# Kernel optimization log

Measured on AMD Instinct MI355X. Metric: run time of the kernel, lower is better.

## Reference

```python
import jax, jax.numpy as jnp
import numpy as np

B, S, H, R = 32, 1024, 1024, 53
EPS = 1e-12
ATT_EPS = 1e10


def setup_inputs() -> dict:
    key = jax.random.key(0)
    ks = jax.random.split(key, 20)
    sc = 0.02
    n = lambda k, shape: jax.random.normal(k, shape, jnp.float32) * sc
    return {
        "relation": jax.random.randint(ks[0], (B, 1), 0, R),
        "last_hidden_size": jax.random.normal(ks[1], (B, S, H), jnp.float32),
        "sub_head": jax.random.randint(ks[2], (B, 1), 0, S),
        "sub_tail": jax.random.randint(ks[3], (B, 1), 0, S),
        "attention_mask": jax.random.randint(ks[4], (B, S), 0, 2).astype(jnp.int32),
        # learned params
        "rel_emb": n(ks[5], (R, H)),
        "Wrf": n(ks[6], (H, H)), "brf": jnp.zeros((H,), jnp.float32),
        "cln_w": jnp.ones((H,), jnp.float32), "cln_b": jnp.zeros((H,), jnp.float32),
        "Wwd": n(ks[7], (H, 2 * H)), "Wbd": n(ks[8], (H, 2 * H)),
        "Wq": n(ks[9], (H, H)), "bq": jnp.zeros((H,), jnp.float32),
        "Wk": n(ks[10], (H, H)), "bk": jnp.zeros((H,), jnp.float32),
        "Wv": n(ks[11], (H, H)), "bv": jnp.zeros((H,), jnp.float32),
        "Wo": n(ks[12], (1, H)), "bo": jnp.zeros((1,), jnp.float32),
    }


def reference(relation, last_hidden_size, sub_head, sub_tail, attention_mask,
              rel_emb, Wrf, brf, cln_w, cln_b, Wwd, Wbd,
              Wq, bq, Wk, bk, Wv, bv, Wo, bo):
    x = last_hidden_size  # [B,S,H]; dropout is identity at inference
    # relation feature: embedding -> linear -> ReLU6
    rel = jnp.clip(jnp.einsum('boh,gh->bog', rel_emb[relation], Wrf) + brf, 0.0, 6.0)  # [B,1,H]
    # gather subject head/tail token features
    bidx = jnp.arange(x.shape[0])[:, None]
    sub = (x[bidx, sub_head] + x[bidx, sub_tail]) * 0.5  # [B,1,H]
    cond = jnp.concatenate([rel, sub], axis=-1)  # [B,1,2H]
    # conditional layer norm: per-example weight/bias generated from cond
    w = jnp.einsum('boc,gc->bog', cond, Wwd) + cln_w  # [B,1,H]
    b = jnp.einsum('boc,gc->bog', cond, Wbd) + cln_b  # [B,1,H]
    mean = jnp.mean(x, axis=-1, keepdims=True)
    c = x - mean
    var = jnp.mean(c * c, axis=-1, keepdims=True)
    normed = c / jnp.sqrt(var + EPS) * w + b  # [B,S,H]
    # ReLU-activated QKV attention with additive mask bias and residual
    q = jax.nn.relu(jnp.einsum('bsh,gh->bsg', normed, Wq) + bq)
    k = jax.nn.relu(jnp.einsum('bsh,gh->bsg', normed, Wk) + bk)
    v = jax.nn.relu(jnp.einsum('bsh,gh->bsg', normed, Wv) + bv)
    e = jnp.einsum('bsh,bth->bst', q, k)  # [B,S,S]
    m = attention_mask.astype(e.dtype)[:, None, :]  # [B,1,S]
    e = e - ATT_EPS * (1.0 - m)
    a = jax.nn.softmax(e, axis=-1)
    hidden = jnp.einsum('bst,bth->bsh', a, v) + normed  # [B,S,H]
    pred_obj_head = (jnp.einsum('bsh,gh->bsg', hidden, Wo) + bo)[..., 0]  # [B,S]
    return (pred_obj_head, hidden)
```

## Files before the change

kernel.cpp:

```cpp
#include <hip/hip_runtime.h>
#include <hip/hip_bf16.h>

#define NB 32
#define NS 1024
#define NH 1024

typedef short s16x4 __attribute__((ext_vector_type(4)));
typedef short s16x8 __attribute__((ext_vector_type(8)));
typedef float f32x4 __attribute__((ext_vector_type(4)));

typedef __attribute__((address_space(3))) void lds_void;
typedef const __attribute__((address_space(1))) void gmem_void;

__device__ __forceinline__ short f2bf(float f) {
  __hip_bfloat16 h = __float2bfloat16(f);
  return *reinterpret_cast<short*>(&h);
}
__device__ __forceinline__ float bf2f(short s) {
  union { unsigned u; float f; } cv;
  cv.u = ((unsigned)(unsigned short)s) << 16;
  return cv.f;
}

__device__ __forceinline__ float wave_reduce_sum(float v) {
#pragma unroll
  for (int o = 32; o; o >>= 1) v += __shfl_xor(v, o);
  return v;
}
__device__ __forceinline__ float wave_reduce_max(float v) {
#pragma unroll
  for (int o = 32; o; o >>= 1) v = fmaxf(v, __shfl_xor(v, o));
  return v;
}
__device__ __forceinline__ float block_reduce_sum(float v, float* red) {
  v = wave_reduce_sum(v);
  __syncthreads();
  if ((threadIdx.x & 63) == 0) red[threadIdx.x >> 6] = v;
  __syncthreads();
  return red[0] + red[1] + red[2] + red[3];
}
__device__ __forceinline__ float block_reduce_max(float v, float* red) {
  v = wave_reduce_max(v);
  __syncthreads();
  if ((threadIdx.x & 63) == 0) red[threadIdx.x >> 6] = v;
  __syncthreads();
  return fmaxf(fmaxf(red[0], red[1]), fmaxf(red[2], red[3]));
}


#define BAR1 do { __builtin_amdgcn_s_barrier();                              \
                  asm volatile("s_waitcnt lgkmcnt(0)" ::: "memory");         \
                  __builtin_amdgcn_sched_barrier(0); } while (0)
#define BAR2 do { __builtin_amdgcn_s_barrier();                              \
                  asm volatile("" ::: "memory"); } while (0)
#define VW   asm volatile("s_waitcnt vmcnt(4)" ::: "memory")
#define VW2  asm volatile("s_waitcnt vmcnt(2)" ::: "memory")

#define GEMM_PRE()                                                           \
  const int tid  = threadIdx.x;                                              \
  const int lane = tid & 63;                                                 \
  const int w    = tid >> 6;                                                 \
  const int wm   = w >> 2, wn = w & 3;                                       \
  const int fr   = lane & 15, fq = lane >> 4;                                \
  const long tA  = (long)(tid >> 3) * 1024 +                                 \
                   (((tid & 7) ^ ((tid >> 3) & 7)) << 3);                    \
  const int kc0  = (fq * 8) ^ ((fr & 7) * 8);                                \
  const int kc1  = (fq * 8 + 32) ^ ((fr & 7) * 8);                           \
  const int rdA  = wm * 8192 + fr * 64;                                      \
  const int rdB  = 16384 + (wn >> 1) * 8192 + (wn & 1) * 4096 + fr * 64;     \
  const int wsl  = w * 512;                                                  \
  f32x4 acc[8][4];                                                           \
  s16x8 aF[2][4][2], bF[2][2][2];                                            \
  _Pragma("unroll") for (int i_ = 0; i_ < 8; ++i_)                           \
    _Pragma("unroll") for (int j_ = 0; j_ < 4; ++j_)                         \
      acc[i_][j_] = (f32x4){0.f, 0.f, 0.f, 0.f};

#define STAGE(d, isB, h, kt)                                                 \
  do {                                                                       \
    const short* _g = ((isB) ? gB + (n0 + (h) * 128) * 1024                  \
                             : gA + (m0 + (h) * 128) * 1024) +               \
                      (long)((kt) & 15) * 64 + tA;                           \
    short* _l = lds + (d) * 32768 + (isB) * 16384 + (h) * 8192 + wsl;        \
    __builtin_amdgcn_global_load_lds((gmem_void*)_g, (lds_void*)_l,          \
                                     16, 0, 0);                              \
    __builtin_amdgcn_global_load_lds((gmem_void*)(_g + 65536),               \
                                     (lds_void*)(_l + 4096), 16, 0, 0);      \
  } while (0)

#define RD_A(d, mq)                                                          \
  _Pragma("unroll") for (int mi = 0; mi < 4; ++mi) {                         \
    aF[mq][mi][0] = *(const s16x8*)(lds + (d) * 32768 + rdA + (mq) * 4096 +  \
                                    mi * 1024 + kc0);                        \
    aF[mq][mi][1] = *(const s16x8*)(lds + (d) * 32768 + rdA + (mq) * 4096 +  \
                                    mi * 1024 + kc1);                        \
  }
#define RD_B(d, nq)                                                          \
  _Pragma("unroll") for (int ni = 0; ni < 2; ++ni) {                         \
    bF[nq][ni][0] = *(const s16x8*)(lds + (d) * 32768 + rdB + (nq) * 2048 +  \
                                    ni * 1024 + kc0);                        \
    bF[nq][ni][1] = *(const s16x8*)(lds + (d) * 32768 + rdB + (nq) * 2048 +  \
                                    ni * 1024 + kc1);                        \
  }
#define MMA(mq, nq)                                                          \
  do {                                                                       \
    __builtin_amdgcn_s_setprio(1);                                           \
    _Pragma("unroll") for (int kk = 0; kk < 2; ++kk)                         \
      _Pragma("unroll") for (int mi = 0; mi < 4; ++mi)                       \
        _Pragma("unroll") for (int ni = 0; ni < 2; ++ni)                     \
          acc[(mq) * 4 + mi][(nq) * 2 + ni] =                                \
              __builtin_amdgcn_mfma_f32_16x16x32_bf16(                       \
                  aF[mq][mi][kk], bF[nq][ni][kk],                            \
                  acc[(mq) * 4 + mi][(nq) * 2 + ni], 0, 0, 0);               \
    __builtin_amdgcn_s_setprio(0);                                           \
  } while (0)

#define GEMM_MAIN()                                                          \
  GEMM_PRE();                                                                \
  STAGE(0, 1, 0, 0); STAGE(0, 1, 1, 0); STAGE(0, 0, 0, 0); STAGE(0, 0, 1, 0);\
  STAGE(1, 1, 0, 1); STAGE(1, 1, 1, 1);                                      \
  VW; BAR2;                                                                  \
  RD_A(0, 0);                                                                \
  for (int it = 0; it < 8; ++it) {                                           \
    const int t1 = 2 * it + 1, t2 = 2 * it + 2, t3 = 2 * it + 3;             \
    RD_B(0, 0); STAGE(1, 0, 0, t1); BAR1; MMA(0, 0); BAR2;                   \
    RD_B(0, 1); STAGE(1, 0, 1, t1); BAR1; MMA(0, 1); BAR2;                   \
    RD_A(0, 1); STAGE(0, 1, 0, t2); BAR1; MMA(1, 1); BAR2;                   \
    VW2;        STAGE(0, 1, 1, t2); BAR1; RD_A(1, 0); MMA(1, 0); BAR2;       \
    RD_B(1, 0); STAGE(0, 0, 0, t2); BAR1; MMA(0, 0); BAR2;                   \
    RD_B(1, 1); STAGE(0, 0, 1, t2); BAR1; MMA(0, 1); BAR2;                   \
    RD_A(1, 1); STAGE(1, 1, 0, t3); BAR1; MMA(1, 1); BAR2;                   \
    VW2;        STAGE(1, 1, 1, t3); BAR1; RD_A(0, 0); MMA(1, 0); BAR2;       \
  }


__global__ __launch_bounds__(256) void prep_kernel(const int* __restrict__ relation,
    const float* __restrict__ x, const int* __restrict__ sub_head,
    const int* __restrict__ sub_tail, const float* __restrict__ rel_emb,
    const float* __restrict__ Wrf, const float* __restrict__ brf,
    float* __restrict__ cond,
    const float* __restrict__ Wq, const float* __restrict__ Wk,
    const float* __restrict__ Wv, short* __restrict__ wout) {
  const int blk = blockIdx.x;
  const int tid = threadIdx.x;
  if (blk >= 1056) {
    long i = ((long)(blk - 1056) * 256 + tid) * 4;
    int seg = (int)(i >> 20);
    long off = i & 1048575;
    const float* src = seg == 0 ? Wq : (seg == 1 ? Wk : Wv);
    f32x4 v = *(const f32x4*)(src + off);
    s16x4 o = { f2bf(v[0]), f2bf(v[1]), f2bf(v[2]), f2bf(v[3]) };
    *(s16x4*)(wout + i) = o;
    return;
  }
  if (blk >= 1024) {
    const int b = blk - 1024;
    const int sh = sub_head[b], st = sub_tail[b];
    for (int h = tid * 4; h < NH; h += 1024) {
      f32x4 a = *(const f32x4*)(x + ((long)b * NS + sh) * NH + h);
      f32x4 c = *(const f32x4*)(x + ((long)b * NS + st) * NH + h);
      f32x4 o = { 0.5f * (a[0] + c[0]), 0.5f * (a[1] + c[1]),
                  0.5f * (a[2] + c[2]), 0.5f * (a[3] + c[3]) };
      *(f32x4*)(cond + b * 2 * NH + NH + h) = o;
    }
    return;
  }
  const int g = blk;
  __shared__ float wr[NH];
  for (int h = tid * 4; h < NH; h += 1024)
    *(f32x4*)(wr + h) = *(const f32x4*)(Wrf + (long)g * NH + h);
  __syncthreads();
  const int lane = tid & 63, wid = tid >> 6;
  const float bg = brf[g];
  for (int b = wid; b < NB; b += 4) {
    const int rid = relation[b];
    const float* re = rel_emb + (long)rid * NH;
    float s = 0.f;
#pragma unroll
    for (int h = lane * 4; h < NH; h += 256) {
      f32x4 rv = *(const f32x4*)(re + h);
      f32x4 wv = *(const f32x4*)(wr + h);
      s += rv[0] * wv[0] + rv[1] * wv[1] + rv[2] * wv[2] + rv[3] * wv[3];
    }
    s = wave_reduce_sum(s);
    if (lane == 0) cond[b * 2 * NH + g] = fminf(fmaxf(s + bg, 0.f), 6.f);
  }
}

__global__ __launch_bounds__(256) void wb_kernel(const float* __restrict__ cond,
    const float* __restrict__ Wwd, const float* __restrict__ Wbd,
    const float* __restrict__ cln_w, const float* __restrict__ cln_b,
    float* __restrict__ wln, float* __restrict__ bln) {
  const int g = blockIdx.x;
  const int tid = threadIdx.x;
  __shared__ float wrow[2 * NH];
  __shared__ float brow[2 * NH];
  for (int i = tid * 4; i < 2 * NH; i += 1024) {
    *(f32x4*)(wrow + i) = *(const f32x4*)(Wwd + (long)g * 2 * NH + i);
    *(f32x4*)(brow + i) = *(const f32x4*)(Wbd + (long)g * 2 * NH + i);
  }
  __syncthreads();
  const int lane = tid & 63, wid = tid >> 6;
  const float cw = cln_w[g], cb = cln_b[g];
  for (int b = wid; b < NB; b += 4) {
    float sw = 0.f, sb = 0.f;
#pragma unroll
    for (int c = lane * 4; c < 2 * NH; c += 256) {
      f32x4 cv = *(const f32x4*)(cond + b * 2 * NH + c);
      f32x4 wv = *(const f32x4*)(wrow + c);
      f32x4 bv = *(const f32x4*)(brow + c);
      sw += cv[0] * wv[0] + cv[1] * wv[1] + cv[2] * wv[2] + cv[3] * wv[3];
      sb += cv[0] * bv[0] + cv[1] * bv[1] + cv[2] * bv[2] + cv[3] * bv[3];
    }
    sw = wave_reduce_sum(sw);
    sb = wave_reduce_sum(sb);
    if (lane == 0) {
      wln[b * NH + g] = sw + cw;
      bln[b * NH + g] = sb + cb;
    }
  }
}

__global__ __launch_bounds__(256) void ln_kernel(const float* __restrict__ x,
    const float* __restrict__ wln, const float* __restrict__ bln, short* __restrict__ normed) {
  const long row = blockIdx.x;
  const int tid = threadIdx.x;
  const long b = row >> 10;
  __shared__ float red[4];
  f32x4 v = *(const f32x4*)(x + row * NH + tid * 4);
  float mean = block_reduce_sum(v[0] + v[1] + v[2] + v[3], red) * (1.f / NH);
  float c0 = v[0] - mean, c1 = v[1] - mean, c2 = v[2] - mean, c3 = v[3] - mean;
  float var = block_reduce_sum(c0 * c0 + c1 * c1 + c2 * c2 + c3 * c3, red) * (1.f / NH);
  float rstd = rsqrtf(var + 1e-12f);
  f32x4 wv = *(const f32x4*)(wln + b * NH + tid * 4);
  f32x4 bv = *(const f32x4*)(bln + b * NH + tid * 4);
  s16x4 o = { f2bf(c0 * rstd * wv[0] + bv[0]), f2bf(c1 * rstd * wv[1] + bv[1]),
              f2bf(c2 * rstd * wv[2] + bv[2]), f2bf(c3 * rstd * wv[3] + bv[3]) };
  *(s16x4*)(normed + row * NH + tid * 4) = o;
}

__global__ __launch_bounds__(512, 2) void qkv_kernel(const short* __restrict__ A,
    const short* __restrict__ Wqkv,
    const float* __restrict__ bq, const float* __restrict__ bk, const float* __restrict__ bv,
    short* __restrict__ q, short* __restrict__ k, short* __restrict__ vT) {
  __shared__ short lds[67584];
  const int flat = blockIdx.y * 12 + blockIdx.x;
  const int gid  = (flat & 7) * 192 + (flat >> 3);
  const int mt = gid / 12, nt = gid % 12;
  const short* gA = A;
  const short* gB = Wqkv;
  const long n0 = (long)nt * 256;
  const long m0 = (long)mt * 256;
  GEMM_MAIN();
  const int z = nt >> 2;
  const long hc0 = (long)(nt & 3) * 256;
  const float* bias = z == 0 ? bq : (z == 1 ? bk : bv);
  if (z < 2) {
    short* dst = z == 0 ? q : k;
#pragma unroll
    for (int nI = 0; nI < 4; ++nI) {
      const long col = hc0 + wn * 64 + nI * 16 + fr;
      const float bcol = bias[col];
#pragma unroll
      for (int mI = 0; mI < 8; ++mI)
#pragma unroll
        for (int r = 0; r < 4; ++r) {
          const long row = m0 + wm * 128 + mI * 16 + fq * 4 + r;
          dst[row * NH + col] = f2bf(fmaxf(acc[mI][nI][r] + bcol, 0.f));
        }
    }
  } else {
    asm volatile("s_waitcnt vmcnt(0)" ::: "memory");
    __syncthreads();
#pragma unroll
    for (int nI = 0; nI < 4; ++nI) {
      const int hl = wn * 64 + nI * 16 + fr;
      const float bcol = bias[hc0 + hl];
#pragma unroll
      for (int mI = 0; mI < 8; ++mI) {
        const int tl = wm * 128 + mI * 16 + fq * 4;
        s16x4 pk = { f2bf(fmaxf(acc[mI][nI][0] + bcol, 0.f)),
                     f2bf(fmaxf(acc[mI][nI][1] + bcol, 0.f)),
                     f2bf(fmaxf(acc[mI][nI][2] + bcol, 0.f)),
                     f2bf(fmaxf(acc[mI][nI][3] + bcol, 0.f)) };
        *(s16x4*)(lds + hl * 264 + tl) = pk;
      }
    }
    __syncthreads();
    const int h = tid >> 1, half = tid & 1;
    const long bb = m0 >> 10;
    short* dst = vT + ((bb * NH) + hc0 + h) * NS + (m0 & 1023) + half * 128;
    const short* src = lds + h * 264 + half * 128;
#pragma unroll
    for (int j = 0; j < 16; ++j)
      *(s16x8*)(dst + j * 8) = *(const s16x8*)(src + j * 8);
  }
}

__global__ __launch_bounds__(512, 2) void escore_kernel(const short* __restrict__ q,
    const short* __restrict__ k, const int* __restrict__ amask, float* __restrict__ e) {
  __shared__ short lds[65536];
  const int flat = blockIdx.z * 16 + blockIdx.y * 4 + blockIdx.x;
  const int gid  = (flat & 7) * 64 + (flat >> 3);
  const int b = gid >> 4, mt = (gid >> 2) & 3, nt = gid & 3;
  const short* gA = q + (long)b * NS * NH;
  const short* gB = k + (long)b * NS * NH;
  const long m0 = (long)mt * 256;
  const long n0 = (long)nt * 256;
  GEMM_MAIN();
  float* eb = e + (long)b * NS * NS;
#pragma unroll
  for (int mI = 0; mI < 8; ++mI)
#pragma unroll
    for (int nI = 0; nI < 4; ++nI) {
      const long col = n0 + wn * 64 + nI * 16 + fr;
      const float mb = -1e10f * (1.f - (float)amask[b * NS + col]);
#pragma unroll
      for (int r = 0; r < 4; ++r) {
        const long row = m0 + wm * 128 + mI * 16 + fq * 4 + r;
        eb[row * NS + col] = acc[mI][nI][r] + mb;
      }
    }
}

__global__ __launch_bounds__(256) void softmax_kernel(const float* __restrict__ e,
    short* __restrict__ a, float* __restrict__ inv_sum) {
  const long row = blockIdx.x;
  const int tid = threadIdx.x;
  __shared__ float red[4];
  f32x4 v = *(const f32x4*)(e + row * NS + tid * 4);
  float m = block_reduce_max(fmaxf(fmaxf(v[0], v[1]), fmaxf(v[2], v[3])), red);
  float p0 = expf(v[0] - m), p1 = expf(v[1] - m);
  float p2 = expf(v[2] - m), p3 = expf(v[3] - m);
  float s = block_reduce_sum(p0 + p1 + p2 + p3, red);
  s16x4 o = { f2bf(p0), f2bf(p1), f2bf(p2), f2bf(p3) };
  *(s16x4*)(a + row * NS + tid * 4) = o;
  if (tid == 0) inv_sum[row] = 1.f / s;
}

__global__ __launch_bounds__(512, 2) void av_kernel(const short* __restrict__ a,
    const short* __restrict__ vT, const float* __restrict__ inv_sum,
    const short* __restrict__ normed, const float* __restrict__ Wo,
    float* __restrict__ hid, float* __restrict__ pred_part) {
  __shared__ short lds[65536];
  const int flat = blockIdx.z * 16 + blockIdx.y * 4 + blockIdx.x;
  const int gid  = (flat & 7) * 64 + (flat >> 3);
  const int b = gid >> 4, mt = (gid >> 2) & 3, nt = gid & 3;
  const short* gA = a + (long)b * NS * NS;
  const short* gB = vT + (long)b * NH * NS;
  const long m0 = (long)mt * 256;
  const long n0 = (long)nt * 256;
  GEMM_MAIN();
  float pp[8][4];
#pragma unroll
  for (int mI = 0; mI < 8; ++mI)
#pragma unroll
    for (int r = 0; r < 4; ++r) pp[mI][r] = 0.f;
#pragma unroll
  for (int nI = 0; nI < 4; ++nI) {
    const long col = n0 + wn * 64 + nI * 16 + fr;
    const float wo = Wo[col];
#pragma unroll
    for (int mI = 0; mI < 8; ++mI)
#pragma unroll
      for (int r = 0; r < 4; ++r) {
        const long row = m0 + wm * 128 + mI * 16 + fq * 4 + r;
        const long gi = ((long)b * NS + row) * NH + col;
        float hv = acc[mI][nI][r] * inv_sum[b * NS + row] + bf2f(normed[gi]);
        hid[gi] = hv;
        pp[mI][r] += hv * wo;
      }
  }
#pragma unroll
  for (int mI = 0; mI < 8; ++mI)
#pragma unroll
    for (int r = 0; r < 4; ++r) {
      float v = pp[mI][r];
      v += __shfl_xor(v, 1);
      v += __shfl_xor(v, 2);
      v += __shfl_xor(v, 4);
      v += __shfl_xor(v, 8);
      if (fr == 0)
        pred_part[((long)nt * 4 + wn) * (NB * NS) + (long)b * NS + m0 +
                  wm * 128 + mI * 16 + fq * 4 + r] = v;
    }
}

__global__ __launch_bounds__(256) void pred_finish_kernel(const float* __restrict__ pp,
    const float* __restrict__ bo, float* __restrict__ pred) {
  const int i = (blockIdx.x * 256 + threadIdx.x) * 4;
  const float bz = bo[0];
  f32x4 o = { bz, bz, bz, bz };
#pragma unroll
  for (int j = 0; j < 16; ++j) {
    f32x4 a = *(const f32x4*)(pp + (long)j * (NB * NS) + i);
    o[0] += a[0]; o[1] += a[1]; o[2] += a[2]; o[3] += a[3];
  }
  *(f32x4*)(pred + i) = o;
}

extern "C" void kernel_launch(void* const* d_in, const int* in_sizes, int n_in,
                              void* d_out, int out_size, void* d_ws, size_t ws_size,
                              hipStream_t stream) {
  (void)in_sizes; (void)n_in; (void)out_size; (void)ws_size;
  const int*   relation = (const int*)d_in[0];
  const float* x        = (const float*)d_in[1];
  const int*   sub_head = (const int*)d_in[2];
  const int*   sub_tail = (const int*)d_in[3];
  const int*   amask    = (const int*)d_in[4];
  const float* rel_emb  = (const float*)d_in[5];
  const float* Wrf      = (const float*)d_in[6];
  const float* brf      = (const float*)d_in[7];
  const float* cln_w    = (const float*)d_in[8];
  const float* cln_b    = (const float*)d_in[9];
  const float* Wwd      = (const float*)d_in[10];
  const float* Wbd      = (const float*)d_in[11];
  const float* Wq       = (const float*)d_in[12];
  const float* bq       = (const float*)d_in[13];
  const float* Wk       = (const float*)d_in[14];
  const float* bk       = (const float*)d_in[15];
  const float* Wv       = (const float*)d_in[16];
  const float* bv       = (const float*)d_in[17];
  const float* Wo       = (const float*)d_in[18];
  const float* bo       = (const float*)d_in[19];

  char* ws = (char*)d_ws;
  short* wqkv_bf = (short*)ws;
  float* cond    = (float*)(ws + 6291456);
  float* wln     = cond + 32 * 2048;
  float* bln     = wln + 32 * 1024;
  float* inv_sum = bln + 32 * 1024;
  short* normed  = (short*)(inv_sum + 32768);
  short* qb      = normed + 33554432;
  short* kb      = qb + 33554432;
  short* vT      = kb + 33554432;
  float* e       = (float*)(vT + 33554432);
  float* pred_part = e + 33554432;

  float* pred = (float*)d_out;
  float* hid  = pred + 32768;

  prep_kernel<<<4128, 256, 0, stream>>>(relation, x, sub_head, sub_tail,
                                        rel_emb, Wrf, brf, cond,
                                        Wq, Wk, Wv, wqkv_bf);
  wb_kernel<<<NH, 256, 0, stream>>>(cond, Wwd, Wbd, cln_w, cln_b, wln, bln);
  ln_kernel<<<NB * NS, 256, 0, stream>>>(x, wln, bln, normed);
  qkv_kernel<<<dim3(12, 128), 512, 0, stream>>>(normed, wqkv_bf,
                                                bq, bk, bv, qb, kb, vT);
  escore_kernel<<<dim3(4, 4, 32), 512, 0, stream>>>(qb, kb, amask, e);
  softmax_kernel<<<NB * NS, 256, 0, stream>>>(e, qb, inv_sum);
  av_kernel<<<dim3(4, 4, 32), 512, 0, stream>>>(qb, vT, inv_sum, normed, Wo,
                                                hid, pred_part);
  pred_finish_kernel<<<32, 256, 0, stream>>>(pred_part, bo, pred);
}
```

Baseline: 520.5 us.

## Store attention scores as fp16 and peel the final GEMM pipeline iteration

The escore kernel now writes masked scores as fp16 instead of fp32, with an offset of -40 and a clamp so values stay in fp16 range. The softmax kernel reads these half-width scores, which halves the traffic of the largest intermediate, the B×S×S score tensor. The GEMM main loop peels its last iteration so the pipeline no longer issues wrap-around prefetches of tile 0. This drops useless loads and the trailing vmcnt wait in the epilogue. The cost is coarser score precision from fp16 rounding and a dependence on the scores staying within the clamped range.

```diff
diff --git a/kernel.cpp b/kernel.cpp
--- a/kernel.cpp
+++ b/kernel.cpp
@@ -1,5 +1,6 @@
 #include <hip/hip_runtime.h>
 #include <hip/hip_bf16.h>
+#include <hip/hip_fp16.h>
 
 #define NB 32
 #define NS 1024
@@ -20,6 +21,14 @@
   union { unsigned u; float f; } cv;
   cv.u = ((unsigned)(unsigned short)s) << 16;
   return cv.f;
+}
+__device__ __forceinline__ short f2h(float f) {
+  __half h = __float2half_rn(f);
+  return *reinterpret_cast<short*>(&h);
+}
+__device__ __forceinline__ float h2f(short s) {
+  __half h = *reinterpret_cast<__half*>(&s);
+  return __half2float(h);
 }
 
 __device__ __forceinline__ float wave_reduce_sum(float v) {
@@ -55,6 +64,7 @@
                   asm volatile("" ::: "memory"); } while (0)
 #define VW   asm volatile("s_waitcnt vmcnt(4)" ::: "memory")
 #define VW2  asm volatile("s_waitcnt vmcnt(2)" ::: "memory")
+#define VW0  asm volatile("s_waitcnt vmcnt(0)" ::: "memory")
 
 #define GEMM_PRE()                                                           \
   const int tid  = threadIdx.x;                                              \
@@ -79,7 +89,7 @@
   do {                                                                       \
     const short* _g = ((isB) ? gB + (n0 + (h) * 128) * 1024                  \
                              : gA + (m0 + (h) * 128) * 1024) +               \
-                      (long)((kt) & 15) * 64 + tA;                           \
+                      (long)(kt) * 64 + tA;                                  \
     short* _l = lds + (d) * 32768 + (isB) * 16384 + (h) * 8192 + wsl;        \
     __builtin_amdgcn_global_load_lds((gmem_void*)_g, (lds_void*)_l,          \
                                      16, 0, 0);                              \
@@ -120,7 +130,7 @@
   STAGE(1, 1, 0, 1); STAGE(1, 1, 1, 1);                                      \
   VW; BAR2;                                                                  \
   RD_A(0, 0);                                                                \
-  for (int it = 0; it < 8; ++it) {                                           \
+  for (int it = 0; it < 7; ++it) {                                           \
     const int t1 = 2 * it + 1, t2 = 2 * it + 2, t3 = 2 * it + 3;             \
     RD_B(0, 0); STAGE(1, 0, 0, t1); BAR1; MMA(0, 0); BAR2;                   \
     RD_B(0, 1); STAGE(1, 0, 1, t1); BAR1; MMA(0, 1); BAR2;                   \
@@ -130,7 +140,16 @@
     RD_B(1, 1); STAGE(0, 0, 1, t2); BAR1; MMA(0, 1); BAR2;                   \
     RD_A(1, 1); STAGE(1, 1, 0, t3); BAR1; MMA(1, 1); BAR2;                   \
     VW2;        STAGE(1, 1, 1, t3); BAR1; RD_A(0, 0); MMA(1, 0); BAR2;       \
-  }
+  }                                                                          \
+     \
+  RD_B(0, 0); STAGE(1, 0, 0, 15); BAR1; MMA(0, 0); BAR2;                     \
+  RD_B(0, 1); STAGE(1, 0, 1, 15); BAR1; MMA(0, 1); BAR2;                     \
+  RD_A(0, 1);                     BAR1; MMA(1, 1); BAR2;                     \
+  VW0;                            BAR1; RD_A(1, 0); MMA(1, 0); BAR2;         \
+  RD_B(1, 0);                     BAR1; MMA(0, 0); BAR2;                     \
+  RD_B(1, 1);                     BAR1; MMA(0, 1); BAR2;                     \
+  RD_A(1, 1);                     BAR1; MMA(1, 1); BAR2;                     \
+  VW0;                            BAR1; MMA(1, 0); BAR2;
 
 
 __global__ __launch_bounds__(256) void prep_kernel(const int* __restrict__ relation,
@@ -269,7 +288,6 @@
         }
     }
   } else {
-    asm volatile("s_waitcnt vmcnt(0)" ::: "memory");
     __syncthreads();
 #pragma unroll
     for (int nI = 0; nI < 4; ++nI) {
@@ -297,7 +315,7 @@
 }
 
 __global__ __launch_bounds__(512, 2) void escore_kernel(const short* __restrict__ q,
-    const short* __restrict__ k, const int* __restrict__ amask, float* __restrict__ e) {
+    const short* __restrict__ k, const int* __restrict__ amask, short* __restrict__ e) {
   __shared__ short lds[65536];
   const int flat = blockIdx.z * 16 + blockIdx.y * 4 + blockIdx.x;
   const int gid  = (flat & 7) * 64 + (flat >> 3);
@@ -307,30 +325,31 @@
   const long m0 = (long)mt * 256;
   const long n0 = (long)nt * 256;
   GEMM_MAIN();
-  float* eb = e + (long)b * NS * NS;
+  short* eb = e + (long)b * NS * NS;
 #pragma unroll
   for (int mI = 0; mI < 8; ++mI)
 #pragma unroll
     for (int nI = 0; nI < 4; ++nI) {
       const long col = n0 + wn * 64 + nI * 16 + fr;
-      const float mb = -1e10f * (1.f - (float)amask[b * NS + col]);
+      const float mb = -1e10f * (1.f - (float)amask[b * NS + col]) - 40.f;
 #pragma unroll
       for (int r = 0; r < 4; ++r) {
         const long row = m0 + wm * 128 + mI * 16 + fq * 4 + r;
-        eb[row * NS + col] = acc[mI][nI][r] + mb;
+        eb[row * NS + col] = f2h(fmaxf(acc[mI][nI][r] + mb, -60000.f));
       }
     }
 }
 
-__global__ __launch_bounds__(256) void softmax_kernel(const float* __restrict__ e,
+__global__ __launch_bounds__(256) void softmax_kernel(const short* __restrict__ e,
     short* __restrict__ a, float* __restrict__ inv_sum) {
   const long row = blockIdx.x;
   const int tid = threadIdx.x;
   __shared__ float red[4];
-  f32x4 v = *(const f32x4*)(e + row * NS + tid * 4);
-  float m = block_reduce_max(fmaxf(fmaxf(v[0], v[1]), fmaxf(v[2], v[3])), red);
-  float p0 = expf(v[0] - m), p1 = expf(v[1] - m);
-  float p2 = expf(v[2] - m), p3 = expf(v[3] - m);
+  s16x4 ev = *(const s16x4*)(e + row * NS + tid * 4);
+  float v0 = h2f(ev[0]), v1 = h2f(ev[1]), v2 = h2f(ev[2]), v3 = h2f(ev[3]);
+  float m = block_reduce_max(fmaxf(fmaxf(v0, v1), fmaxf(v2, v3)), red);
+  float p0 = expf(v0 - m), p1 = expf(v1 - m);
+  float p2 = expf(v2 - m), p3 = expf(v3 - m);
   float s = block_reduce_sum(p0 + p1 + p2 + p3, red);
   s16x4 o = { f2bf(p0), f2bf(p1), f2bf(p2), f2bf(p3) };
   *(s16x4*)(a + row * NS + tid * 4) = o;
@@ -433,8 +452,8 @@
   short* qb      = normed + 33554432;
   short* kb      = qb + 33554432;
   short* vT      = kb + 33554432;
-  float* e       = (float*)(vT + 33554432);
-  float* pred_part = e + 33554432;
+  short* e       = vT + 33554432;
+  float* pred_part = (float*)(e + 33554432);
 
   float* pred = (float*)d_out;
   float* hid  = pred + 32768;
```

Result: faster. 499.1 us (-4.1%).
